# Performance work log

Hardware: AMD Instinct MI355X
Metric: run time of the kernel (lower is better)

The kernel has to match this reference:

```python
import jax, jax.numpy as jnp
import numpy as np

B, T, C, H = 2, 2048, 1024, 16
D = C // H  # head_dim = 64


def setup_inputs() -> dict:
    key = jax.random.key(0)
    k1, k2, k3 = jax.random.split(key, 3)
    x = jax.random.normal(k1, (B, T, C), dtype=jnp.float32)
    Wqkv = jax.random.normal(k2, (C, 3 * C), dtype=jnp.float32) * (1.0 / np.sqrt(C))
    Wo = jax.random.normal(k3, (C, C), dtype=jnp.float32) * (1.0 / np.sqrt(C))
    bo = jnp.zeros((C,), dtype=jnp.float32)
    return {"x": x, "Wqkv": Wqkv, "Wo": Wo, "bo": bo}


def reference(x, Wqkv, Wo, bo):
    Bc, Tc, Cc = x.shape
    qkv = x @ Wqkv                                  # [B,T,3C]
    q, k, v = jnp.split(qkv, 3, axis=-1)
    # [B,T,C] -> [B,H,T,D]
    q = q.reshape(Bc, Tc, H, D).transpose(0, 2, 1, 3)
    k = k.reshape(Bc, Tc, H, D).transpose(0, 2, 1, 3)
    v = v.reshape(Bc, Tc, H, D).transpose(0, 2, 1, 3)
    scale = 1.0 / np.sqrt(D)
    att = jnp.einsum('bhqd,bhkd->bhqk', q, k) * scale   # [B,H,T,T]
    causal = jnp.tril(jnp.ones((Tc, Tc), dtype=bool))
    att = jnp.where(causal[None, None], att, -jnp.inf)
    att = jax.nn.softmax(att, axis=-1)
    # dropout treated as identity (eval mode)
    y = jnp.einsum('bhqk,bhkd->bhqd', att, v)           # [B,H,T,D]
    y = y.transpose(0, 2, 1, 3).reshape(Bc, Tc, Cc)     # [B,T,C]
    return y @ Wo + bo
```

## Files before the change

### kernel.cpp

```cpp
#include <hip/hip_runtime.h>
#include <hip/hip_bf16.h>
#include <math.h>


typedef __attribute__((ext_vector_type(8))) short bf16x8;
typedef __attribute__((ext_vector_type(4))) float f32x4;

__device__ __forceinline__ float b2f(unsigned short u) {
    union { unsigned int i; float f; } x; x.i = ((unsigned int)u) << 16; return x.f;
}
__device__ __forceinline__ unsigned short f2b(float f) {
    __hip_bfloat16 h = __float2bfloat16(f);
    return *reinterpret_cast<unsigned short*>(&h);
}
__device__ __forceinline__ unsigned short f2b_rz(float f) {
    union { float f; unsigned int i; } u; u.f = f; return (unsigned short)(u.i >> 16);
}
__device__ __forceinline__ float fexp2(float x) {
#if __has_builtin(__builtin_amdgcn_exp2f)
    return __builtin_amdgcn_exp2f(x);
#else
    return exp2f(x);
#endif
}
__device__ __forceinline__ void gload_lds16(const void* g, void* l) {
    __builtin_amdgcn_global_load_lds(
        (__attribute__((address_space(1))) void*)g,
        (__attribute__((address_space(3))) void*)l, 16, 0, 0);
}

__device__ __forceinline__ void transpose_job(
        const void* __restrict__ in, unsigned short* __restrict__ out,
        int R, int Cc, int use_bf, int nscale, float scale,
        int c0, int r0, int tid, unsigned short (*t)[33]) {
    const unsigned short* inb = (const unsigned short*)in;
    const float* inf = (const float*)in;
    const int x = tid & 31, y = (tid >> 5) & 7;
    #pragma unroll
    for (int i = 0; i < 32; i += 8) {
        size_t idx = (size_t)(r0 + y + i) * Cc + c0 + x;
        float v = use_bf ? b2f(inb[idx]) : inf[idx];
        if (c0 + x < nscale) v *= scale;
        t[y + i][x] = f2b(v);
    }
    __syncthreads();
    #pragma unroll
    for (int i = 0; i < 32; i += 8)
        out[(size_t)(c0 + y + i) * R + r0 + x] = t[x][y + i];
}

__global__ __launch_bounds__(256) void prep_kernel(
        const void* __restrict__ xin, const void* __restrict__ Wqkv,
        const void* __restrict__ Wo, const void* __restrict__ bias,
        unsigned short* __restrict__ xb, unsigned short* __restrict__ WqkvT,
        unsigned short* __restrict__ WoT, unsigned short* __restrict__ bob,
        int* __restrict__ flag, float qscale) {
    __shared__ __align__(16) unsigned short t[32][33];
    __shared__ int det;
    const int tid = threadIdx.x, blk = blockIdx.x;

    if (tid < 64) {
        const unsigned short* xu = (const unsigned short*)xin;
        int cnt = 0;
        for (int i = tid; i < 1024; i += 64) {
            unsigned short u = xu[2 * i];
            int e = (u >> 7) & 0xFF;
            if (!((e == 0) || (e >= 96 && e <= 159))) cnt++;
        }
        #pragma unroll
        for (int m = 1; m < 64; m <<= 1) cnt += __shfl_xor(cnt, m);
        if (tid == 0) det = (cnt > 200) ? 0 : 1;
    }
    __syncthreads();
    const int use_bf = det;

    if (blk < 4096) {
        int i4 = blk * 1024 + tid * 4;
        if (use_bf) {
            *(ushort4*)(xb + i4) = *(const ushort4*)((const unsigned short*)xin + i4);
        } else {
            float4 f = *(const float4*)((const float*)xin + i4);
            ushort4 o;
            o.x = f2b(f.x); o.y = f2b(f.y); o.z = f2b(f.z); o.w = f2b(f.w);
            *(ushort4*)(xb + i4) = o;
        }
    } else if (blk < 7168) {
        int tt = blk - 4096;
        int c0 = (tt % 96) * 32, r0 = (tt / 96) * 32;
        transpose_job(Wqkv, WqkvT, 1024, 3072, use_bf, 1024, qscale, c0, r0, tid, t);
    } else if (blk < 8192) {
        int tt = blk - 7168;
        int c0 = (tt & 31) * 32, r0 = (tt >> 5) * 32;
        transpose_job(Wo, WoT, 1024, 1024, use_bf, 0, 1.0f, c0, r0, tid, t);
    } else {
        int i4 = tid * 4;
        if (use_bf) {
            *(ushort4*)(bob + i4) = *(const ushort4*)((const unsigned short*)bias + i4);
        } else {
            float4 f = *(const float4*)((const float*)bias + i4);
            ushort4 o;
            o.x = f2b(f.x); o.y = f2b(f.y); o.z = f2b(f.z); o.w = f2b(f.w);
            *(ushort4*)(bob + i4) = o;
        }
        if (tid == 0) *flag = use_bf;
    }
}

__global__ __launch_bounds__(256) void gemm_qkv(
        const unsigned short* __restrict__ A, const unsigned short* __restrict__ Bt,
        unsigned short* __restrict__ qb, unsigned short* __restrict__ kb,
        unsigned short* __restrict__ vt) {
    __shared__ __align__(16) unsigned short lA[128 * 64];
    __shared__ __align__(16) unsigned short lB[128 * 64];
    const int tid  = threadIdx.x;
    const int wave = tid >> 6, lane = tid & 63;
    const int g = lane >> 4, c = lane & 15;
    const int m0 = blockIdx.y * 128, n0 = blockIdx.x * 128;
    const int wm = (wave & 1) * 64, wn = (wave >> 1) * 64;
    const int srow = lane >> 3;
    const int sc8  = ((lane & 7) ^ ((lane >> 3) & 7)) * 8;

    f32x4 acc[4][4] = {};

    for (int k0 = 0; k0 < 1024; k0 += 64) {
        #pragma unroll
        for (int i = 0; i < 4; i++) {
            int seg = wave * 4 + i;
            int row = seg * 8 + srow;
            gload_lds16(A  + (size_t)(m0 + row) * 1024 + k0 + sc8, lA + seg * 512);
            gload_lds16(Bt + (size_t)(n0 + row) * 1024 + k0 + sc8, lB + seg * 512);
        }
        __syncthreads();

        #pragma unroll
        for (int dk = 0; dk < 2; dk++) {
            const int off = ((4 * dk + g) ^ (c & 7)) << 3;
            bf16x8 af[4], bfv[4];
            #pragma unroll
            for (int i = 0; i < 4; i++) {
                af[i]  = *(const bf16x8*)(lA + (wm + 16 * i + c) * 64 + off);
                bfv[i] = *(const bf16x8*)(lB + (wn + 16 * i + c) * 64 + off);
            }
            #pragma unroll
            for (int mi = 0; mi < 4; mi++)
                #pragma unroll
                for (int ni = 0; ni < 4; ni++)
                    acc[mi][ni] = __builtin_amdgcn_mfma_f32_16x16x32_bf16(
                        af[mi], bfv[ni], acc[mi][ni], 0, 0, 0);
        }
        __syncthreads();
    }

    const int colbase = n0 + wn;
    if (colbase < 2048) {
        unsigned short* dst = (colbase < 1024) ? qb : kb;
        int cb = colbase & 1023;
        #pragma unroll
        for (int mi = 0; mi < 4; mi++)
            #pragma unroll
            for (int ni = 0; ni < 4; ni++)
                #pragma unroll
                for (int r = 0; r < 4; r++) {
                    int row = m0 + wm + 16 * mi + 4 * g + r;
                    dst[(size_t)row * 1024 + cb + 16 * ni + c] = f2b(acc[mi][ni][r]);
                }
    } else {
        const int bb = m0 >> 11;
        const int kvb = (m0 & 2047) + wm;
        #pragma unroll
        for (int mi = 0; mi < 4; mi++)
            #pragma unroll
            for (int ni = 0; ni < 4; ni++) {
                int dg = colbase + 16 * ni + c - 2048;
                int bh = bb * 16 + (dg >> 6);
                int kv = kvb + 16 * mi + 4 * g;
                ushort4 pk;
                pk.x = f2b(acc[mi][ni][0]); pk.y = f2b(acc[mi][ni][1]);
                pk.z = f2b(acc[mi][ni][2]); pk.w = f2b(acc[mi][ni][3]);
                *(ushort4*)(vt + ((size_t)bh * 64 + (dg & 63)) * 2048 + kv) = pk;
            }
    }
}

__global__ __launch_bounds__(256) void gemm_nt(
        const unsigned short* __restrict__ A, const unsigned short* __restrict__ Bt,
        void* __restrict__ C, const unsigned short* __restrict__ bias,
        const int* __restrict__ out_f32_flag, int M, int N, int K) {
    __shared__ __align__(16) unsigned short lA[128 * 64];
    __shared__ __align__(16) unsigned short lB[128 * 64];
    const int tid  = threadIdx.x;
    const int wave = tid >> 6, lane = tid & 63;
    const int g = lane >> 4, c = lane & 15;
    const int m0 = blockIdx.y * 128, n0 = blockIdx.x * 128;
    const int wm = (wave & 1) * 64, wn = (wave >> 1) * 64;
    const int srow = lane >> 3;
    const int sc8  = ((lane & 7) ^ ((lane >> 3) & 7)) * 8;

    f32x4 acc[4][4] = {};

    for (int k0 = 0; k0 < K; k0 += 64) {
        #pragma unroll
        for (int i = 0; i < 4; i++) {
            int seg = wave * 4 + i;
            int row = seg * 8 + srow;
            gload_lds16(A  + (size_t)(m0 + row) * K + k0 + sc8, lA + seg * 512);
            gload_lds16(Bt + (size_t)(n0 + row) * K + k0 + sc8, lB + seg * 512);
        }
        __syncthreads();

        #pragma unroll
        for (int dk = 0; dk < 2; dk++) {
            const int off = ((4 * dk + g) ^ (c & 7)) << 3;
            bf16x8 af[4], bfv[4];
            #pragma unroll
            for (int i = 0; i < 4; i++) {
                af[i]  = *(const bf16x8*)(lA + (wm + 16 * i + c) * 64 + off);
                bfv[i] = *(const bf16x8*)(lB + (wn + 16 * i + c) * 64 + off);
            }
            #pragma unroll
            for (int mi = 0; mi < 4; mi++)
                #pragma unroll
                for (int ni = 0; ni < 4; ni++)
                    acc[mi][ni] = __builtin_amdgcn_mfma_f32_16x16x32_bf16(
                        af[mi], bfv[ni], acc[mi][ni], 0, 0, 0);
        }
        __syncthreads();
    }

    const bool f32out = out_f32_flag && (*out_f32_flag == 0);
    #pragma unroll
    for (int mi = 0; mi < 4; mi++)
        #pragma unroll
        for (int ni = 0; ni < 4; ni++)
            #pragma unroll
            for (int r = 0; r < 4; r++) {
                int row = m0 + wm + 16 * mi + 4 * g + r;
                int col = n0 + wn + 16 * ni + c;
                float v = acc[mi][ni][r];
                if (bias) v += b2f(bias[col]);
                if (f32out) ((float*)C)[(size_t)row * N + col] = v;
                else ((unsigned short*)C)[(size_t)row * N + col] = f2b(v);
            }
}

template<bool MASKED>
__device__ __forceinline__ void tile_compute(
        const unsigned short* __restrict__ lKs, const unsigned short* __restrict__ lVts,
        unsigned short* __restrict__ P, const bf16x8* qB, f32x4* o,
        float& l_run, int wave, int lane, int g, int c) {
    const f32x4 sinit = {-12.f, -12.f, -12.f, -12.f};
    f32x4 s[4] = {sinit, sinit, sinit, sinit};
    #pragma unroll
    for (int nt = 0; nt < 4; nt++)
        #pragma unroll
        for (int dk = 0; dk < 2; dk++) {
            bf16x8 kA = *(const bf16x8*)(lKs + (16 * nt + c) * 64 + (((4 * dk + g) ^ (c & 7)) << 3));
            s[nt] = __builtin_amdgcn_mfma_f32_16x16x32_bf16(kA, qB[dk], s[nt], 0, 0, 0);
        }

    float rsum = 0.f;
    #pragma unroll
    for (int nt = 0; nt < 4; nt++) {
        unsigned int pk0 = 0, pk1 = 0;
        #pragma unroll
        for (int r = 0; r < 4; r++) {
            float v = s[nt][r];
            if (MASKED) v = (16 * nt + 4 * g + r <= 16 * wave + c) ? v : -1e30f;
            float p = fexp2(v);
            rsum += p;
            unsigned int pb = f2b_rz(p);
            if (r == 0) pk0 = pb;
            else if (r == 1) pk0 |= pb << 16;
            else if (r == 2) pk1 = pb;
            else pk1 |= pb << 16;
        }
        int kvl = 16 * nt + 4 * g;
        int base = c * 64 + (((kvl >> 3) ^ (c & 7)) << 3) + (kvl & 7);
        *(unsigned int*)(P + base)     = pk0;
        *(unsigned int*)(P + base + 2) = pk1;
    }
    rsum += __shfl_xor(rsum, 16);
    rsum += __shfl_xor(rsum, 32);
    l_run += rsum;

    __asm__ volatile("s_waitcnt lgkmcnt(0)" ::: "memory");

    bf16x8 pf[2];
    #pragma unroll
    for (int kk = 0; kk < 2; kk++)
        pf[kk] = *(const bf16x8*)(P + c * 64 + (((4 * kk + g) ^ (c & 7)) << 3));
    #pragma unroll
    for (int ni = 0; ni < 4; ni++)
        #pragma unroll
        for (int kk = 0; kk < 2; kk++) {
            bf16x8 vf = *(const bf16x8*)(lVts + (16 * ni + c) * 64 + (((4 * kk + g) ^ (c & 7)) << 3));
            o[ni] = __builtin_amdgcn_mfma_f32_16x16x32_bf16(pf[kk], vf, o[ni], 0, 0, 0);
        }
    __asm__ volatile("" ::: "memory");
}

__global__ __launch_bounds__(256) void attn_kernel(
        const unsigned short* __restrict__ qb, const unsigned short* __restrict__ kb,
        const unsigned short* __restrict__ vt, unsigned short* __restrict__ Y) {
    __shared__ __align__(16) unsigned short lK[2][4096];
    __shared__ __align__(16) unsigned short lVt[2][4096];
    __shared__ __align__(16) unsigned short Pbuf[4][1024];

    const int tid = threadIdx.x, wave = tid >> 6, lane = tid & 63;
    const int g = lane >> 4, c = lane & 15;
    unsigned short* P = Pbuf[wave];
    const int srow = lane >> 3;
    const int sc8  = ((lane & 7) ^ ((lane >> 3) & 7)) * 8;

    const int rr = blockIdx.x >> 8, cc = blockIdx.x & 255;
    const int kslot = cc >> 3;
    const int j  = (rr & 1) ? kslot : (31 - kslot);
    const int bh = rr * 8 + (cc & 7);
    const int q0 = j * 64;
    const int b = bh >> 4, h = bh & 15;
    const int rbase = q0 + 16 * wave;

    const unsigned short* Qb  = qb + (size_t)b * 2048 * 1024 + h * 64;
    const unsigned short* Kb  = kb + (size_t)b * 2048 * 1024 + h * 64;
    const unsigned short* Vtb = vt + (size_t)bh * 64 * 2048;

    bf16x8 qB[2];
    #pragma unroll
    for (int dk = 0; dk < 2; dk++)
        qB[dk] = *(const bf16x8*)(Qb + (size_t)(rbase + c) * 1024 + 32 * dk + 8 * g);

    f32x4 o[4] = {};
    float l_run = 0.f;

    #pragma unroll 1
    for (int kv0 = 0; kv0 <= q0; kv0 += 128) {
        const bool do1 = (kv0 + 64 <= q0);
        #pragma unroll
        for (int i = 0; i < 2; i++) {
            int seg = wave * 2 + i;
            int row = seg * 8 + srow;
            gload_lds16(Kb  + (size_t)(kv0 + row) * 1024 + sc8, lK[0] + seg * 512);
            gload_lds16(Vtb + (size_t)row * 2048 + kv0 + sc8,   lVt[0] + seg * 512);
            if (do1) {
                gload_lds16(Kb  + (size_t)(kv0 + 64 + row) * 1024 + sc8, lK[1] + seg * 512);
                gload_lds16(Vtb + (size_t)row * 2048 + kv0 + 64 + sc8,   lVt[1] + seg * 512);
            }
        }
        __syncthreads();

        if (kv0 == q0)
            tile_compute<true >(lK[0], lVt[0], P, qB, o, l_run, wave, lane, g, c);
        else
            tile_compute<false>(lK[0], lVt[0], P, qB, o, l_run, wave, lane, g, c);
        if (do1) {
            if (kv0 + 64 == q0)
                tile_compute<true >(lK[1], lVt[1], P, qB, o, l_run, wave, lane, g, c);
            else
                tile_compute<false>(lK[1], lVt[1], P, qB, o, l_run, wave, lane, g, c);
        }
        __syncthreads();
    }

    float inv = 1.f / l_run;
    float il[4];
    #pragma unroll
    for (int r = 0; r < 4; r++)
        il[r] = __shfl(inv, (lane & 48) | (4 * g + r));
    #pragma unroll
    for (int ni = 0; ni < 4; ni++)
        #pragma unroll
        for (int r = 0; r < 4; r++) {
            int row = rbase + 4 * g + r;
            Y[(size_t)(b * 2048 + row) * 1024 + h * 64 + 16 * ni + c] =
                f2b(o[ni][r] * il[r]);
        }
}

extern "C" void kernel_launch(void* const* d_in, const int* in_sizes, int n_in,
                              void* d_out, int out_size, void* d_ws, size_t ws_size,
                              hipStream_t stream) {
    char* ws = (char*)d_ws;
    unsigned short* qb    = (unsigned short*)(ws);
    unsigned short* kb    = (unsigned short*)(ws + 8388608);
    unsigned short* vt    = (unsigned short*)(ws + 16777216);
    unsigned short* Y     = (unsigned short*)(ws + 25165824);
    unsigned short* WqkvT = (unsigned short*)(ws + 33554432);
    unsigned short* WoT   = (unsigned short*)(ws + 39845888);
    unsigned short* xb    = (unsigned short*)(ws + 41943040);
    unsigned short* bob   = (unsigned short*)(ws + 50331648);
    int*            flag  = (int*)(ws + 50333696);

    prep_kernel<<<8193, 256, 0, stream>>>(
        d_in[0], d_in[1], d_in[2], d_in[3], xb, WqkvT, WoT, bob, flag,
        0.125f * 1.4426950408889634f);

    gemm_qkv<<<dim3(24, 32), 256, 0, stream>>>(xb, WqkvT, qb, kb, vt);

    attn_kernel<<<1024, 256, 0, stream>>>(qb, kb, vt, Y);

    gemm_nt<<<dim3(8, 32), 256, 0, stream>>>(Y, WoT, d_out, bob, flag, 4096, 1024, 1024);
}
```

Before: 196.7 us.

## Enlarge prep transpose tiles, halve output GEMM tile width, pack P stores

The prep kernel now uses 64x64 transpose tiles and has each block convert 4096 elements of x, cutting the grid from 8193 to 2049 blocks and reducing per-block overhead. The output projection GEMM switches from 128x128 to 128x64 tiles with 4 waves stacked along M, doubling the grid to 512 blocks so the 256 CUs are better filled. The attention P-tile writes are merged into a single 64-bit LDS store. The trade-offs are less reuse of B per block in the GEMM and a larger LDS tile in prep.

```diff
diff --git a/kernel.cpp b/kernel.cpp
--- a/kernel.cpp
+++ b/kernel.cpp
@@ -29,15 +29,15 @@
         (__attribute__((address_space(3))) void*)l, 16, 0, 0);
 }
 
-__device__ __forceinline__ void transpose_job(
+__device__ __forceinline__ void transpose_job64(
         const void* __restrict__ in, unsigned short* __restrict__ out,
-        int R, int Cc, int use_bf, int nscale, float scale,
-        int c0, int r0, int tid, unsigned short (*t)[33]) {
+        int Cc, int use_bf, int nscale, float scale,
+        int c0, int r0, int tid, unsigned short (*t)[65]) {
     const unsigned short* inb = (const unsigned short*)in;
     const float* inf = (const float*)in;
-    const int x = tid & 31, y = (tid >> 5) & 7;
-    #pragma unroll
-    for (int i = 0; i < 32; i += 8) {
+    const int x = tid & 63, y = tid >> 6;
+    #pragma unroll
+    for (int i = 0; i < 64; i += 4) {
         size_t idx = (size_t)(r0 + y + i) * Cc + c0 + x;
         float v = use_bf ? b2f(inb[idx]) : inf[idx];
         if (c0 + x < nscale) v *= scale;
@@ -45,8 +45,8 @@
     }
     __syncthreads();
     #pragma unroll
-    for (int i = 0; i < 32; i += 8)
-        out[(size_t)(c0 + y + i) * R + r0 + x] = t[x][y + i];
+    for (int i = 0; i < 64; i += 4)
+        out[(size_t)(c0 + y + i) * 1024 + r0 + x] = t[x][y + i];
 }
 
 __global__ __launch_bounds__(256) void prep_kernel(
@@ -55,7 +55,7 @@
         unsigned short* __restrict__ xb, unsigned short* __restrict__ WqkvT,
         unsigned short* __restrict__ WoT, unsigned short* __restrict__ bob,
         int* __restrict__ flag, float qscale) {
-    __shared__ __align__(16) unsigned short t[32][33];
+    __shared__ __align__(16) unsigned short t[64][65];
     __shared__ int det;
     const int tid = threadIdx.x, blk = blockIdx.x;
 
@@ -74,24 +74,28 @@
     __syncthreads();
     const int use_bf = det;
 
-    if (blk < 4096) {
-        int i4 = blk * 1024 + tid * 4;
-        if (use_bf) {
-            *(ushort4*)(xb + i4) = *(const ushort4*)((const unsigned short*)xin + i4);
-        } else {
-            float4 f = *(const float4*)((const float*)xin + i4);
-            ushort4 o;
-            o.x = f2b(f.x); o.y = f2b(f.y); o.z = f2b(f.z); o.w = f2b(f.w);
-            *(ushort4*)(xb + i4) = o;
-        }
-    } else if (blk < 7168) {
-        int tt = blk - 4096;
-        int c0 = (tt % 96) * 32, r0 = (tt / 96) * 32;
-        transpose_job(Wqkv, WqkvT, 1024, 3072, use_bf, 1024, qscale, c0, r0, tid, t);
-    } else if (blk < 8192) {
-        int tt = blk - 7168;
-        int c0 = (tt & 31) * 32, r0 = (tt >> 5) * 32;
-        transpose_job(Wo, WoT, 1024, 1024, use_bf, 0, 1.0f, c0, r0, tid, t);
+    if (blk < 1024) {
+        int base = blk * 4096;
+        #pragma unroll
+        for (int i = 0; i < 4; i++) {
+            int i4 = base + (tid + 256 * i) * 4;
+            if (use_bf) {
+                *(ushort4*)(xb + i4) = *(const ushort4*)((const unsigned short*)xin + i4);
+            } else {
+                float4 f = *(const float4*)((const float*)xin + i4);
+                ushort4 o;
+                o.x = f2b(f.x); o.y = f2b(f.y); o.z = f2b(f.z); o.w = f2b(f.w);
+                *(ushort4*)(xb + i4) = o;
+            }
+        }
+    } else if (blk < 1792) {
+        int tt = blk - 1024;
+        int c0 = (tt % 48) * 64, r0 = (tt / 48) * 64;
+        transpose_job64(Wqkv, WqkvT, 3072, use_bf, 1024, qscale, c0, r0, tid, t);
+    } else if (blk < 2048) {
+        int tt = blk - 1792;
+        int c0 = (tt & 15) * 64, r0 = (tt >> 4) * 64;
+        transpose_job64(Wo, WoT, 1024, use_bf, 0, 1.0f, c0, r0, tid, t);
     } else {
         int i4 = tid * 4;
         if (use_bf) {
@@ -187,23 +191,28 @@
         void* __restrict__ C, const unsigned short* __restrict__ bias,
         const int* __restrict__ out_f32_flag, int M, int N, int K) {
     __shared__ __align__(16) unsigned short lA[128 * 64];
-    __shared__ __align__(16) unsigned short lB[128 * 64];
+    __shared__ __align__(16) unsigned short lB[64 * 64];
     const int tid  = threadIdx.x;
     const int wave = tid >> 6, lane = tid & 63;
     const int g = lane >> 4, c = lane & 15;
-    const int m0 = blockIdx.y * 128, n0 = blockIdx.x * 128;
-    const int wm = (wave & 1) * 64, wn = (wave >> 1) * 64;
+    const int m0 = blockIdx.y * 128, n0 = blockIdx.x * 64;
+    const int wm = wave * 32;
     const int srow = lane >> 3;
     const int sc8  = ((lane & 7) ^ ((lane >> 3) & 7)) * 8;
 
-    f32x4 acc[4][4] = {};
+    f32x4 acc[2][4] = {};
 
     for (int k0 = 0; k0 < K; k0 += 64) {
         #pragma unroll
         for (int i = 0; i < 4; i++) {
             int seg = wave * 4 + i;
             int row = seg * 8 + srow;
-            gload_lds16(A  + (size_t)(m0 + row) * K + k0 + sc8, lA + seg * 512);
+            gload_lds16(A + (size_t)(m0 + row) * K + k0 + sc8, lA + seg * 512);
+        }
+        #pragma unroll
+        for (int i = 0; i < 2; i++) {
+            int seg = wave * 2 + i;
+            int row = seg * 8 + srow;
             gload_lds16(Bt + (size_t)(n0 + row) * K + k0 + sc8, lB + seg * 512);
         }
         __syncthreads();
@@ -211,14 +220,15 @@
         #pragma unroll
         for (int dk = 0; dk < 2; dk++) {
             const int off = ((4 * dk + g) ^ (c & 7)) << 3;
-            bf16x8 af[4], bfv[4];
-            #pragma unroll
-            for (int i = 0; i < 4; i++) {
+            bf16x8 af[2], bfv[4];
+            #pragma unroll
+            for (int i = 0; i < 2; i++)
                 af[i]  = *(const bf16x8*)(lA + (wm + 16 * i + c) * 64 + off);
-                bfv[i] = *(const bf16x8*)(lB + (wn + 16 * i + c) * 64 + off);
-            }
-            #pragma unroll
-            for (int mi = 0; mi < 4; mi++)
+            #pragma unroll
+            for (int i = 0; i < 4; i++)
+                bfv[i] = *(const bf16x8*)(lB + (16 * i + c) * 64 + off);
+            #pragma unroll
+            for (int mi = 0; mi < 2; mi++)
                 #pragma unroll
                 for (int ni = 0; ni < 4; ni++)
                     acc[mi][ni] = __builtin_amdgcn_mfma_f32_16x16x32_bf16(
@@ -229,13 +239,13 @@
 
     const bool f32out = out_f32_flag && (*out_f32_flag == 0);
     #pragma unroll
-    for (int mi = 0; mi < 4; mi++)
+    for (int mi = 0; mi < 2; mi++)
         #pragma unroll
         for (int ni = 0; ni < 4; ni++)
             #pragma unroll
             for (int r = 0; r < 4; r++) {
                 int row = m0 + wm + 16 * mi + 4 * g + r;
-                int col = n0 + wn + 16 * ni + c;
+                int col = n0 + 16 * ni + c;
                 float v = acc[mi][ni][r];
                 if (bias) v += b2f(bias[col]);
                 if (f32out) ((float*)C)[(size_t)row * N + col] = v;
@@ -261,23 +271,17 @@
     float rsum = 0.f;
     #pragma unroll
     for (int nt = 0; nt < 4; nt++) {
-        unsigned int pk0 = 0, pk1 = 0;
+        unsigned long long pk = 0;
         #pragma unroll
         for (int r = 0; r < 4; r++) {
             float v = s[nt][r];
             if (MASKED) v = (16 * nt + 4 * g + r <= 16 * wave + c) ? v : -1e30f;
             float p = fexp2(v);
             rsum += p;
-            unsigned int pb = f2b_rz(p);
-            if (r == 0) pk0 = pb;
-            else if (r == 1) pk0 |= pb << 16;
-            else if (r == 2) pk1 = pb;
-            else pk1 |= pb << 16;
+            pk |= ((unsigned long long)f2b_rz(p)) << (16 * r);
         }
         int kvl = 16 * nt + 4 * g;
-        int base = c * 64 + (((kvl >> 3) ^ (c & 7)) << 3) + (kvl & 7);
-        *(unsigned int*)(P + base)     = pk0;
-        *(unsigned int*)(P + base + 2) = pk1;
+        *(unsigned long long*)(P + c * 64 + (((kvl >> 3) ^ (c & 7)) << 3) + (kvl & 7)) = pk;
     }
     rsum += __shfl_xor(rsum, 16);
     rsum += __shfl_xor(rsum, 32);
@@ -390,7 +394,7 @@
     unsigned short* bob   = (unsigned short*)(ws + 50331648);
     int*            flag  = (int*)(ws + 50333696);
 
-    prep_kernel<<<8193, 256, 0, stream>>>(
+    prep_kernel<<<2049, 256, 0, stream>>>(
         d_in[0], d_in[1], d_in[2], d_in[3], xb, WqkvT, WoT, bob, flag,
         0.125f * 1.4426950408889634f);
 
@@ -398,5 +402,5 @@
 
     attn_kernel<<<1024, 256, 0, stream>>>(qb, kb, vt, Y);
 
-    gemm_nt<<<dim3(8, 32), 256, 0, stream>>>(Y, WoT, d_out, bob, flag, 4096, 1024, 1024);
-}
+    gemm_nt<<<dim3(16, 32), 256, 0, stream>>>(Y, WoT, d_out, bob, flag, 4096, 1024, 1024);
+}
```

After: 187.1 us. -4.9%, faster.
